# Optimization experiments

Measured on AMD Instinct MI355X. Metric: run time of the kernel, lower is better.

## Reference

```python
import jax, jax.numpy as jnp
import numpy as np
import math

D_MODEL = 768
N_HEADS = 12
D_HEAD = D_MODEL // N_HEADS
B, T = 2, 2048


def setup_inputs() -> dict:
    key = jax.random.key(0)
    k1, k2, k3, k4, k5 = jax.random.split(key, 5)
    x = jax.random.normal(k1, (B, T, D_MODEL), dtype=jnp.float32)
    # mask == 1 means masked (masked_fill). Causal: mask upper triangle.
    mask = jnp.triu(jnp.ones((T, T), dtype=jnp.int32), k=1)[None, None]  # [1,1,T,T]
    # qkv Linear: weight [3*d_model, d_model], bias [3*d_model]
    lim_qkv = 1.0 / math.sqrt(D_MODEL)
    W_qkv = jax.random.uniform(k2, (3 * D_MODEL, D_MODEL), minval=-lim_qkv, maxval=lim_qkv, dtype=jnp.float32)
    b_qkv = jax.random.uniform(k3, (3 * D_MODEL,), minval=-lim_qkv, maxval=lim_qkv, dtype=jnp.float32)
    W_proj = jax.random.uniform(k4, (D_MODEL, D_MODEL), minval=-lim_qkv, maxval=lim_qkv, dtype=jnp.float32)
    b_proj = jax.random.uniform(k5, (D_MODEL,), minval=-lim_qkv, maxval=lim_qkv, dtype=jnp.float32)
    return {"x": x, "mask": mask, "W_qkv": W_qkv, "b_qkv": b_qkv, "W_proj": W_proj, "b_proj": b_proj}


def reference(x, mask, W_qkv, b_qkv, W_proj, b_proj):
    Bx, Tx, C = x.shape
    qkv = x @ W_qkv.T + b_qkv                      # [B,T,3C]
    q, k, v = jnp.split(qkv, 3, axis=-1)
    # [B,T,H,Dh] -> [B,H,T,Dh]
    q = q.reshape(Bx, Tx, N_HEADS, D_HEAD).transpose(0, 2, 1, 3)
    k = k.reshape(Bx, Tx, N_HEADS, D_HEAD).transpose(0, 2, 1, 3)
    v = v.reshape(Bx, Tx, N_HEADS, D_HEAD).transpose(0, 2, 1, 3)
    att = jnp.einsum('bhqd,bhkd->bhqk', q, k) / math.sqrt(D_HEAD)
    att = jnp.where(mask == 1, -jnp.inf, att)
    att = jax.nn.softmax(att, axis=-1)
    out = jnp.einsum('bhqk,bhkd->bhqd', att, v)    # [B,H,T,Dh]
    out = out.transpose(0, 2, 1, 3).reshape(Bx, Tx, C)
    return out @ W_proj.T + b_proj
```

## Files before the change

### kernel.cpp

```cpp
#include <hip/hip_runtime.h>
#include <hip/hip_bf16.h>
#include <cstdint>

#define D_MODEL 768
#define N_HEADS 12
#define D_HEAD  64
#define BATCH   2
#define SEQ     2048
#define NQ64    (SEQ / 64)
#define SCALE_Q 0.18033688011112042f
#define NSL     4

typedef float f32x4 __attribute__((ext_vector_type(4)));
typedef short s16x8 __attribute__((ext_vector_type(8)));
typedef short s16x4 __attribute__((ext_vector_type(4)));
typedef unsigned short u16;

static __device__ __forceinline__ u16 f2bf(float f) {
    union { float f; unsigned int u; } c; c.f = f;
    unsigned int u = c.u;
    u += 0x7fffu + ((u >> 16) & 1u);
    return (u16)(u >> 16);
}
static __device__ __forceinline__ float b2f(u16 u) {
    union { unsigned u; float f; } c; c.u = ((unsigned)u) << 16; return c.f;
}
static __device__ __forceinline__ float e2(float x) {
#if __has_builtin(__builtin_amdgcn_exp2f)
    return __builtin_amdgcn_exp2f(x);
#else
    return exp2f(x);
#endif
}
static __device__ __forceinline__ s16x4 pk4(float p0, float p1, float p2, float p3) {
    union { __hip_bfloat162 h[2]; s16x4 v; } u;
    u.h[0] = __float22bfloat162_rn(make_float2(p0, p1));
    u.h[1] = __float22bfloat162_rn(make_float2(p2, p3));
    return u.v;
}

static __device__ __forceinline__ f32x4 mfma16x32(s16x8 a, s16x8 b, f32x4 c) {
    return __builtin_amdgcn_mfma_f32_16x16x32_bf16(a, b, c, 0, 0, 0);
}
static __device__ __forceinline__ f32x4 mfma16x16(s16x4 a, s16x4 b, f32x4 c) {
#if __has_builtin(__builtin_amdgcn_mfma_f32_16x16x16bf16_1k)
    return __builtin_amdgcn_mfma_f32_16x16x16bf16_1k(a, b, c, 0, 0, 0);
#else
    asm volatile("v_mfma_f32_16x16x16_bf16 %0, %1, %2, %0" : "+v"(c) : "v"(a), "v"(b));
    return c;
#endif
}
static __device__ __forceinline__ void gload_lds16(const void* g, void* l) {
    __builtin_amdgcn_global_load_lds(
        (const __attribute__((address_space(1))) unsigned int*)g,
        (__attribute__((address_space(3))) unsigned int*)l, 16, 0, 0);
}

__global__ __launch_bounds__(256)
void cvt3_kernel(const float* __restrict__ s0, u16* __restrict__ d0, int n0,
                 const float* __restrict__ s1, u16* __restrict__ d1, int n1,
                 const float* __restrict__ s2, u16* __restrict__ d2, int n2)
{
    const int idx4 = (blockIdx.x * 256 + threadIdx.x) * 4;
    const float* s; u16* d; int local;
    if (idx4 < n0)           { s = s0; d = d0; local = idx4; }
    else if (idx4 < n0 + n1) { s = s1; d = d1; local = idx4 - n0; }
    else if (idx4 < n0 + n1 + n2) { s = s2; d = d2; local = idx4 - n0 - n1; }
    else return;
    float4 v = *(const float4*)(s + local);
    ushort4 o;
    o.x = f2bf(v.x); o.y = f2bf(v.y); o.z = f2bf(v.z); o.w = f2bf(v.w);
    *(ushort4*)(d + local) = o;
}

template<int BM, int BN, int MODE>
__global__ __launch_bounds__(256)
void mfma_gemm_kernel(const u16* __restrict__ A, const u16* __restrict__ Bw,
                      const float* __restrict__ bias,
                      float* __restrict__ outf,
                      u16* __restrict__ qo, u16* __restrict__ ko, u16* __restrict__ vt,
                      int M, int N, int K)
{
    constexpr int BK = 32;
    __shared__ u16 As[BM * BK];
    __shared__ u16 Bs[BN * BK];
    const int tid = threadIdx.x;
    const int wave = tid >> 6, lane = tid & 63;
    const int wr = wave >> 1, wc = wave & 1;
    constexpr int WM = BM / 2, WN = BN / 2, FI = WM / 16, FJ = WN / 16;
    const int g = lane >> 4, c = lane & 15;
    const int bm = blockIdx.x * BM, bn = blockIdx.y * BN;

    f32x4 acc[FI][FJ] = {};

    constexpr int IA = (BM * BK * 2) / (256 * 16);
    constexpr int IB = (BN * BK * 2) / (256 * 16);

    const u16* asrc[IA]; const u16* bsrc[IB];
    #pragma unroll
    for (int i = 0; i < IA; ++i) {
        const int idx = tid + i * 256;
        const int row = idx >> 2, kc = idx & 3;
        const int kcs = kc ^ ((row >> 1) & 3);
        asrc[i] = A + (size_t)(bm + row) * K + kcs * 8;
    }
    #pragma unroll
    for (int i = 0; i < IB; ++i) {
        const int idx = tid + i * 256;
        const int row = idx >> 2, kc = idx & 3;
        const int kcs = kc ^ ((row >> 1) & 3);
        bsrc[i] = Bw + (size_t)(bn + row) * K + kcs * 8;
    }
    const int gsw = g ^ ((c >> 1) & 3);

    for (int k0 = 0; k0 < K; k0 += BK) {
        if (k0) __syncthreads();
        #pragma unroll
        for (int i = 0; i < IA; ++i) gload_lds16(asrc[i] + k0, &As[(tid + i * 256) * 8]);
        #pragma unroll
        for (int i = 0; i < IB; ++i) gload_lds16(bsrc[i] + k0, &Bs[(tid + i * 256) * 8]);
        __syncthreads();

        s16x8 af[FI], bfr[FJ];
        #pragma unroll
        for (int i = 0; i < FI; ++i)
            af[i] = *(const s16x8*)&As[(wr * WM + i * 16 + c) * BK + gsw * 8];
        #pragma unroll
        for (int j = 0; j < FJ; ++j)
            bfr[j] = *(const s16x8*)&Bs[(wc * WN + j * 16 + c) * BK + gsw * 8];
        #pragma unroll
        for (int i = 0; i < FI; ++i)
            #pragma unroll
            for (int j = 0; j < FJ; ++j)
                acc[i][j] = mfma16x32(af[i], bfr[j], acc[i][j]);
    }

    if (MODE == 1) {
        #pragma unroll
        for (int j = 0; j < FJ; ++j) {
            const int col = bn + wc * WN + j * 16 + c;
            const float bv = bias[col];
            #pragma unroll
            for (int i = 0; i < FI; ++i) {
                const int row0 = bm + wr * WM + i * 16 + g * 4;
                #pragma unroll
                for (int r = 0; r < 4; ++r)
                    outf[(size_t)(row0 + r) * N + col] = acc[i][j][r] + bv;
            }
        }
    } else {
        const int which = bn / D_MODEL;
        #pragma unroll
        for (int j = 0; j < FJ; ++j) {
            const int gcol = bn + wc * WN + j * 16 + c;
            const float bv = bias[gcol];
            const int scol = gcol - which * D_MODEL;
            const int h = scol >> 6, d = scol & 63;
            if (which == 2) {
                #pragma unroll
                for (int i = 0; i < FI; ++i) {
                    const int row0 = bm + wr * WM + i * 16 + g * 4;
                    const int b = row0 >> 11, t = row0 & 2047;
                    ushort4 pv;
                    pv.x = f2bf(acc[i][j][0] + bv);
                    pv.y = f2bf(acc[i][j][1] + bv);
                    pv.z = f2bf(acc[i][j][2] + bv);
                    pv.w = f2bf(acc[i][j][3] + bv);
                    *(ushort4*)(vt + ((size_t)(b * N_HEADS + h) * 64 + d) * SEQ + t) = pv;
                }
            } else {
                u16* dst = (which == 0) ? qo : ko;
                const float sc = (which == 0) ? SCALE_Q : 1.0f;
                #pragma unroll
                for (int i = 0; i < FI; ++i) {
                    const int row0 = bm + wr * WM + i * 16 + g * 4;
                    const int b = row0 >> 11, t = row0 & 2047;
                    #pragma unroll
                    for (int r = 0; r < 4; ++r)
                        dst[(((size_t)(b * N_HEADS + h) * SEQ + t + r) << 6) + d] =
                            f2bf((acc[i][j][r] + bv) * sc);
                }
            }
        }
    }
}

__global__ __launch_bounds__(256, 3)
void mfma_attn_kernel(const u16* __restrict__ qb, const u16* __restrict__ kb,
                      const u16* __restrict__ vtb, u16* __restrict__ ob)
{
    __shared__ __align__(16) u16 OL[NSL][64][64];
    __shared__ float ML[NSL][2][64];
    const int tid = threadIdx.x;
    const int lane = tid & 63;
    const int s = tid >> 6;
    const int blk = blockIdx.x;
    const int bh = blk % (BATCH * N_HEADS);
    const int q = blk / (BATCH * N_HEADS);
    const int jblk = (q <= 10) ? (q + 21) : (q <= 20) ? (31 - q) : (q - 21);

    const int nq = jblk + 1;
    const int t0 = s * nq;
    const int t1 = t0 + nq;
    const int jq0 = 4 * jblk;

    const int g = lane >> 4, c = lane & 15;
    const int rbase = g << 2;
    const int q0 = jblk << 6;

    s16x8 qa0[4], qa1[4];
    #pragma unroll
    for (int qq = 0; qq < 4; ++qq) {
        const u16* qp = qb + ((size_t)bh * SEQ + q0 + qq * 16 + c) * 64 + g * 8;
        qa0[qq] = *(const s16x8*)(qp);
        qa1[qq] = *(const s16x8*)(qp + 32);
    }

    f32x4 o[4][4] = {};
    float m[4] = {0.f, 0.f, 0.f, 0.f};
    float l[4] = {0.f, 0.f, 0.f, 0.f};

#define TILEQ(QQ, CK0, CK1, CV0, CV1, CV2, CV3, MASKED) {                         \
    f32x4 sa = {0,0,0,0}, sb = {0,0,0,0};                                         \
    sa = mfma16x32(CK0, qa0[QQ], sa);                                             \
    sb = mfma16x32(CK1, qa1[QQ], sb);                                             \
    f32x4 sv = sa + sb;                                                           \
    if (MASKED) {                                                                 \
        if (rbase + 0 > c) sv[0] = -1e30f;                                        \
        if (rbase + 1 > c) sv[1] = -1e30f;                                        \
        if (rbase + 2 > c) sv[2] = -1e30f;                                        \
        if (rbase + 3 > c) sv[3] = -1e30f;                                        \
    }                                                                             \
    float pmax = fmaxf(fmaxf(sv[0], sv[1]), fmaxf(sv[2], sv[3]));                 \
    if (__any(pmax > m[QQ] + 8.f)) {                      \
        pmax = fmaxf(pmax, __shfl_xor(pmax, 16));                                 \
        pmax = fmaxf(pmax, __shfl_xor(pmax, 32));                                 \
        const float mn = fmaxf(m[QQ], pmax);                                      \
        const float scr = e2(m[QQ] - mn);                                         \
        l[QQ] *= scr;                                                             \
        f32x4 scv;                                                                \
        scv[0] = __shfl(scr, rbase + 0);                                          \
        scv[1] = __shfl(scr, rbase + 1);                                          \
        scv[2] = __shfl(scr, rbase + 2);                                          \
        scv[3] = __shfl(scr, rbase + 3);                                          \
        o[QQ][0] *= scv; o[QQ][1] *= scv; o[QQ][2] *= scv; o[QQ][3] *= scv;       \
        m[QQ] = mn;                                                               \
    }                                                                             \
    const float p0 = e2(sv[0] - m[QQ]), p1 = e2(sv[1] - m[QQ]);                   \
    const float p2 = e2(sv[2] - m[QQ]), p3 = e2(sv[3] - m[QQ]);                   \
    l[QQ] += (p0 + p1) + (p2 + p3);                                               \
    const s16x4 pa = pk4(p0, p1, p2, p3);                                         \
    o[QQ][0] = mfma16x16(pa, CV0, o[QQ][0]);                                      \
    o[QQ][1] = mfma16x16(pa, CV1, o[QQ][1]);                                      \
    o[QQ][2] = mfma16x16(pa, CV2, o[QQ][2]);                                      \
    o[QQ][3] = mfma16x16(pa, CV3, o[QQ][3]);                                      \
}

    {
        const u16* kp = kb + (size_t)bh * SEQ * 64 + c * 64 + g * 8 + (size_t)t0 * 1024;
        const u16* vp = vtb + ((size_t)bh * 64 + c) * SEQ + g * 4 + t0 * 16;

        s16x8 ck0 = *(const s16x8*)(kp);
        s16x8 ck1 = *(const s16x8*)(kp + 32);
        s16x4 cv0 = *(const s16x4*)(vp);
        s16x4 cv1 = *(const s16x4*)(vp + 16 * SEQ);
        s16x4 cv2 = *(const s16x4*)(vp + 32 * SEQ);
        s16x4 cv3 = *(const s16x4*)(vp + 48 * SEQ);

        for (int t = t0; t < t1; ++t) {
            kp += 1024; vp += 16;
            const s16x8 nk0 = *(const s16x8*)(kp);
            const s16x8 nk1 = *(const s16x8*)(kp + 32);
            const s16x4 nv0 = *(const s16x4*)(vp);
            const s16x4 nv1 = *(const s16x4*)(vp + 16 * SEQ);
            const s16x4 nv2 = *(const s16x4*)(vp + 32 * SEQ);
            const s16x4 nv3 = *(const s16x4*)(vp + 48 * SEQ);

            #pragma unroll
            for (int qq = 0; qq < 4; ++qq) {
                if (t <= jq0 + qq) {
                    TILEQ(qq, ck0, ck1, cv0, cv1, cv2, cv3, (t == jq0 + qq));
                }
            }
            ck0 = nk0; ck1 = nk1;
            cv0 = nv0; cv1 = nv1; cv2 = nv2; cv3 = nv3;
        }
    }
#undef TILEQ

    u16* OLs = &OL[s][0][0];
    #pragma unroll
    for (int qq = 0; qq < 4; ++qq) {
        float lt = l[qq] + __shfl_xor(l[qq], 16);
        lt += __shfl_xor(lt, 32);
        #pragma unroll
        for (int r = 0; r < 4; ++r) {
            const int row = qq * 16 + rbase + r;
            #pragma unroll
            for (int j = 0; j < 4; ++j) {
                const int col = c + 16 * j;
                const int idx = row * 64 + ((((col >> 3) ^ (row & 7)) << 3) | (col & 7));
                OLs[idx] = f2bf(o[qq][j][r]);
            }
        }
        if (g == 0) {
            ML[s][0][qq * 16 + c] = m[qq];
            ML[s][1][qq * 16 + c] = lt;
        }
    }
    __syncthreads();

    {
        const int row = tid >> 2;
        const int cq = (tid & 3) << 4;
        float mv[NSL], lv[NSL];
        float mm = -3.0e38f;
        #pragma unroll
        for (int sp = 0; sp < NSL; ++sp) {
            mv[sp] = ML[sp][0][row];
            lv[sp] = ML[sp][1][row];
            mm = fmaxf(mm, mv[sp]);
        }
        float w[NSL], denom = 0.f;
        #pragma unroll
        for (int sp = 0; sp < NSL; ++sp) {
            w[sp] = e2(mv[sp] - mm);
            denom += lv[sp] * w[sp];
        }
        const float inv = 1.0f / denom;

        float a[16] = {};
        #pragma unroll
        for (int sp = 0; sp < NSL; ++sp) {
            const float ws = w[sp] * inv;
            #pragma unroll
            for (int h2 = 0; h2 < 2; ++h2) {
                const int ch = (cq >> 3) + h2;
                const int idx = row * 64 + ((ch ^ (row & 7)) << 3);
                const uint4 xv = *(const uint4*)&OL[sp][0][idx];
                a[h2 * 8 + 0] += ws * b2f((u16)(xv.x & 0xffff));
                a[h2 * 8 + 1] += ws * b2f((u16)(xv.x >> 16));
                a[h2 * 8 + 2] += ws * b2f((u16)(xv.y & 0xffff));
                a[h2 * 8 + 3] += ws * b2f((u16)(xv.y >> 16));
                a[h2 * 8 + 4] += ws * b2f((u16)(xv.z & 0xffff));
                a[h2 * 8 + 5] += ws * b2f((u16)(xv.z >> 16));
                a[h2 * 8 + 6] += ws * b2f((u16)(xv.w & 0xffff));
                a[h2 * 8 + 7] += ws * b2f((u16)(xv.w >> 16));
            }
        }

        const int b = bh / N_HEADS, h = bh % N_HEADS;
        const int t = (jblk << 6) + row;
        u16* dst = ob + ((size_t)b * SEQ + t) * D_MODEL + h * 64 + cq;
        #pragma unroll
        for (int e4 = 0; e4 < 4; ++e4) {
            ushort4 ov;
            ov.x = f2bf(a[e4 * 4 + 0]);
            ov.y = f2bf(a[e4 * 4 + 1]);
            ov.z = f2bf(a[e4 * 4 + 2]);
            ov.w = f2bf(a[e4 * 4 + 3]);
            *(ushort4*)(dst + e4 * 4) = ov;
        }
    }
}

extern "C" void kernel_launch(void* const* d_in, const int* in_sizes, int n_in,
                              void* d_out, int out_size, void* d_ws, size_t ws_size,
                              hipStream_t stream)
{
    const float* x      = (const float*)d_in[0];
    const float* W_qkv  = (const float*)d_in[2];
    const float* b_qkv  = (const float*)d_in[3];
    const float* W_proj = (const float*)d_in[4];
    const float* b_proj = (const float*)d_in[5];
    float* out = (float*)d_out;

    const int nX = BATCH * SEQ * D_MODEL;
    const int nWq = 3 * D_MODEL * D_MODEL;
    const int nWp = D_MODEL * D_MODEL;
    u16* xb  = (u16*)d_ws;
    u16* wqb = xb + nX;
    u16* wpb = wqb + nWq;
    u16* qbf = wpb + nWp;
    u16* kbf = qbf + nX;
    u16* vtb = kbf + nX;
    u16* ao  = vtb + nX;

    const int tot4 = (nX + nWq + nWp) / 4;
    cvt3_kernel<<<(tot4 + 255) / 256, 256, 0, stream>>>(x, xb, nX, W_qkv, wqb, nWq,
                                                        W_proj, wpb, nWp);

    mfma_gemm_kernel<128, 128, 0><<<dim3(32, 18), 256, 0, stream>>>(
        xb, wqb, b_qkv, nullptr, qbf, kbf, vtb, BATCH * SEQ, 3 * D_MODEL, D_MODEL);

    mfma_attn_kernel<<<dim3(NQ64 * BATCH * N_HEADS), 256, 0, stream>>>(
        qbf, kbf, vtb, ao);

    mfma_gemm_kernel<128, 64, 1><<<dim3(32, 12), 256, 0, stream>>>(
        ao, wpb, b_proj, out, nullptr, nullptr, nullptr, BATCH * SEQ, D_MODEL, D_MODEL);
}
```

Measured before the change: 96.50 us.

## Split long causal attention query blocks across two workgroups with a merge kernel

```diff
diff --git a/kernel.cpp b/kernel.cpp
--- a/kernel.cpp
+++ b/kernel.cpp
@@ -10,6 +10,7 @@
 #define NQ64    (SEQ / 64)
 #define SCALE_Q 0.18033688011112042f
 #define NSL     4
+#define NBH     (BATCH * N_HEADS)
 
 typedef float f32x4 __attribute__((ext_vector_type(4)));
 typedef short s16x8 __attribute__((ext_vector_type(8)));
@@ -187,7 +188,8 @@
 
 __global__ __launch_bounds__(256, 3)
 void mfma_attn_kernel(const u16* __restrict__ qb, const u16* __restrict__ kb,
-                      const u16* __restrict__ vtb, u16* __restrict__ ob)
+                      const u16* __restrict__ vtb, u16* __restrict__ ob,
+                      u16* __restrict__ pO, float* __restrict__ pML)
 {
     __shared__ __align__(16) u16 OL[NSL][64][64];
     __shared__ float ML[NSL][2][64];
@@ -195,13 +197,17 @@
     const int lane = tid & 63;
     const int s = tid >> 6;
     const int blk = blockIdx.x;
-    const int bh = blk % (BATCH * N_HEADS);
-    const int q = blk / (BATCH * N_HEADS);
-    const int jblk = (q <= 10) ? (q + 21) : (q <= 20) ? (31 - q) : (q - 21);
-
-    const int nq = jblk + 1;
-    const int t0 = s * nq;
-    const int t1 = t0 + nq;
+    const int bh = blk % NBH;
+    const int u = blk / NBH;
+    int jblk, half, nparts;
+    if (u < 16) { jblk = 15 - u;          half = 0;          nparts = 1; }
+    else        { const int uu = u - 16;  jblk = 31 - (uu >> 1); half = uu & 1; nparts = 2; }
+
+    const int ntt = 4 * (jblk + 1);
+    const int hl  = ntt / nparts;
+    const int w0  = half * hl;
+    const int t0  = w0 + (hl * s) / 4;
+    const int t1  = w0 + (hl * (s + 1)) / 4;
     const int jq0 = 4 * jblk;
 
     const int g = lane >> 4, c = lane & 15;
@@ -327,12 +333,11 @@
             w[sp] = e2(mv[sp] - mm);
             denom += lv[sp] * w[sp];
         }
-        const float inv = 1.0f / denom;
 
         float a[16] = {};
         #pragma unroll
         for (int sp = 0; sp < NSL; ++sp) {
-            const float ws = w[sp] * inv;
+            const float ws = w[sp];
             #pragma unroll
             for (int h2 = 0; h2 < 2; ++h2) {
                 const int ch = (cq >> 3) + h2;
@@ -349,18 +354,77 @@
             }
         }
 
-        const int b = bh / N_HEADS, h = bh % N_HEADS;
-        const int t = (jblk << 6) + row;
-        u16* dst = ob + ((size_t)b * SEQ + t) * D_MODEL + h * 64 + cq;
-        #pragma unroll
-        for (int e4 = 0; e4 < 4; ++e4) {
-            ushort4 ov;
-            ov.x = f2bf(a[e4 * 4 + 0]);
-            ov.y = f2bf(a[e4 * 4 + 1]);
-            ov.z = f2bf(a[e4 * 4 + 2]);
-            ov.w = f2bf(a[e4 * 4 + 3]);
-            *(ushort4*)(dst + e4 * 4) = ov;
-        }
+        if (nparts == 1) {
+            const float inv = 1.0f / denom;
+            const int b = bh / N_HEADS, h = bh % N_HEADS;
+            const int t = (jblk << 6) + row;
+            u16* dst = ob + ((size_t)b * SEQ + t) * D_MODEL + h * 64 + cq;
+            #pragma unroll
+            for (int e4 = 0; e4 < 4; ++e4) {
+                ushort4 ov;
+                ov.x = f2bf(a[e4 * 4 + 0] * inv);
+                ov.y = f2bf(a[e4 * 4 + 1] * inv);
+                ov.z = f2bf(a[e4 * 4 + 2] * inv);
+                ov.w = f2bf(a[e4 * 4 + 3] * inv);
+                *(ushort4*)(dst + e4 * 4) = ov;
+            }
+        } else {
+            const int ps = (bh * 16 + (jblk - 16)) * 2 + half;
+            u16* Od = pO + (size_t)ps * 4096 + row * 64 + cq;
+            #pragma unroll
+            for (int e4 = 0; e4 < 4; ++e4) {
+                ushort4 ov;
+                ov.x = f2bf(a[e4 * 4 + 0]);
+                ov.y = f2bf(a[e4 * 4 + 1]);
+                ov.z = f2bf(a[e4 * 4 + 2]);
+                ov.w = f2bf(a[e4 * 4 + 3]);
+                *(ushort4*)(Od + e4 * 4) = ov;
+            }
+            if ((tid & 3) == 0) {
+                pML[ps * 128 + row]      = mm;
+                pML[ps * 128 + 64 + row] = denom;
+            }
+        }
+    }
+}
+
+__global__ __launch_bounds__(256)
+void attn_merge_kernel(const u16* __restrict__ pO, const float* __restrict__ pML,
+                       u16* __restrict__ ob)
+{
+    const int blk = blockIdx.x;
+    const int bh = blk % NBH;
+    const int hj = blk / NBH;
+    const int jblk = 16 + hj;
+    const int tid = threadIdx.x;
+    const int row = tid >> 2;
+    const int cq = (tid & 3) << 4;
+    const int ps = (bh * 16 + hj) * 2;
+
+    const float m0 = pML[(size_t)ps * 128 + row];
+    const float l0 = pML[(size_t)ps * 128 + 64 + row];
+    const float m1 = pML[(size_t)(ps + 1) * 128 + row];
+    const float l1 = pML[(size_t)(ps + 1) * 128 + 64 + row];
+    const float mm = fmaxf(m0, m1);
+    const float w0 = e2(m0 - mm), w1 = e2(m1 - mm);
+    const float inv = 1.0f / (l0 * w0 + l1 * w1);
+    const float a0 = w0 * inv, a1 = w1 * inv;
+
+    const u16* O0 = pO + (size_t)ps * 4096 + row * 64 + cq;
+    const u16* O1 = O0 + 4096;
+    const int b = bh / N_HEADS, h = bh % N_HEADS;
+    const int t = (jblk << 6) + row;
+    u16* dst = ob + ((size_t)b * SEQ + t) * D_MODEL + h * 64 + cq;
+    #pragma unroll
+    for (int e4 = 0; e4 < 4; ++e4) {
+        const ushort4 x0 = *(const ushort4*)(O0 + e4 * 4);
+        const ushort4 x1 = *(const ushort4*)(O1 + e4 * 4);
+        ushort4 ov;
+        ov.x = f2bf(a0 * b2f(x0.x) + a1 * b2f(x1.x));
+        ov.y = f2bf(a0 * b2f(x0.y) + a1 * b2f(x1.y));
+        ov.z = f2bf(a0 * b2f(x0.z) + a1 * b2f(x1.z));
+        ov.w = f2bf(a0 * b2f(x0.w) + a1 * b2f(x1.w));
+        *(ushort4*)(dst + e4 * 4) = ov;
     }
 }
 
@@ -385,6 +449,8 @@
     u16* kbf = qbf + nX;
     u16* vtb = kbf + nX;
     u16* ao  = vtb + nX;
+    u16* pO  = ao + nX;
+    float* pML = (float*)(pO + (size_t)768 * 4096);
 
     const int tot4 = (nX + nWq + nWp) / 4;
     cvt3_kernel<<<(tot4 + 255) / 256, 256, 0, stream>>>(x, xb, nX, W_qkv, wqb, nWq,
@@ -393,8 +459,9 @@
     mfma_gemm_kernel<128, 128, 0><<<dim3(32, 18), 256, 0, stream>>>(
         xb, wqb, b_qkv, nullptr, qbf, kbf, vtb, BATCH * SEQ, 3 * D_MODEL, D_MODEL);
 
-    mfma_attn_kernel<<<dim3(NQ64 * BATCH * N_HEADS), 256, 0, stream>>>(
-        qbf, kbf, vtb, ao);
+    mfma_attn_kernel<<<dim3(48 * NBH), 256, 0, stream>>>(
+        qbf, kbf, vtb, ao, pO, pML);
+    attn_merge_kernel<<<dim3(16 * NBH), 256, 0, stream>>>(pO, pML, ao);
 
     mfma_gemm_kernel<128, 64, 1><<<dim3(32, 12), 256, 0, stream>>>(
         ao, wpb, b_proj, out, nullptr, nullptr, nullptr, BATCH * SEQ, D_MODEL, D_MODEL);
```

Measured after the change: 103.7 us. 1.07x slower.
